# Optimization experiments

Measured on AMD Instinct MI355X. Metric: run time of the kernel, lower is better.

## Reference

```python
import jax, jax.numpy as jnp
import numpy as np
from jax import lax

B, C, H, W = 1, 128, 56, 56
NH, NG, KS = 4, 1, 3
CG = C // NG          # channels per group
CH = C // NH          # channels per head
NHG = NH // NG        # heads per group
SCALE = CH ** -0.5


def _norm_grid(h, w, n):
    # matches _get_normalized_grid: (y, x) order, each normalized to [-1, 1]
    y = jnp.arange(h, dtype=jnp.float32) / (h - 1.0) * 2.0 - 1.0
    x = jnp.arange(w, dtype=jnp.float32) / (w - 1.0) * 2.0 - 1.0
    g = jnp.stack(jnp.meshgrid(y, x, indexing='ij'), axis=-1)  # (h, w, 2)
    return jnp.broadcast_to(g[None], (n, h, w, 2))


def _grid_sample(img, grid):
    # F.grid_sample: bilinear, align_corners=True, zeros padding; grid is (x, y) in [-1, 1]
    n, c, hi, wi = img.shape
    gs = grid.shape[1:-1]
    gx = grid[..., 0].reshape(n, -1)
    gy = grid[..., 1].reshape(n, -1)
    fx = (gx + 1.0) * 0.5 * (wi - 1)
    fy = (gy + 1.0) * 0.5 * (hi - 1)
    x0 = jnp.floor(fx)
    y0 = jnp.floor(fy)
    wx = fx - x0
    wy = fy - y0
    x0 = x0.astype(jnp.int32)
    y0 = y0.astype(jnp.int32)
    imgf = img.reshape(n, c, hi * wi)

    def corner(xi, yi, wgt):
        valid = (xi >= 0) & (xi < wi) & (yi >= 0) & (yi < hi)
        idx = jnp.clip(yi, 0, hi - 1) * wi + jnp.clip(xi, 0, wi - 1)
        vals = jax.vmap(lambda im, ii: jnp.take(im, ii, axis=1))(imgf, idx)  # (n, c, P)
        return vals * (wgt * valid)[:, None, :]

    out = (corner(x0, y0, (1 - wx) * (1 - wy)) + corner(x0 + 1, y0, wx * (1 - wy))
           + corner(x0, y0 + 1, (1 - wx) * wy) + corner(x0 + 1, y0 + 1, wx * wy))
    return out.reshape((n, c) + gs)


def _conv1x1(t, w, b):
    return jnp.einsum('bchw,oc->bohw', t, w) + b[None, :, None, None]


def _forward(x, query, dw_w, dw_b, ln_w, ln_b, pw_w, k_w, k_b, v_w, v_b, out_w, out_b, rpe_table):
    # conv_offset: depthwise 3x3 (stride 1, pad 1) -> channel LayerNorm -> GELU -> 1x1 to 2ch (no bias)
    qg = query.reshape(B * NG, CG, H, W)
    t = lax.conv_general_dilated(qg, dw_w, (1, 1), ((1, 1), (1, 1)),
                                 dimension_numbers=('NCHW', 'OIHW', 'NCHW'),
                                 feature_group_count=CG) + dw_b[None, :, None, None]
    mu = t.mean(axis=1, keepdims=True)
    var = ((t - mu) ** 2).mean(axis=1, keepdims=True)
    t = (t - mu) / jnp.sqrt(var + 1e-5) * ln_w[None, :, None, None] + ln_b[None, :, None, None]
    t = jax.nn.gelu(t, approximate=False)
    offset = jnp.einsum('bchw,oc->bohw', t, pw_w)  # (BG, 2, Hk, Wk) in (y, x) order
    Hk, Wk = offset.shape[-2:]
    n_sample = Hk * Wk

    # tanh-scaled offsets (scale_offset_range=True, factor 0.5)
    rng = jnp.array([1.0 / (Hk - 1.0), 1.0 / (Wk - 1.0)], jnp.float32).reshape(1, 2, 1, 1)
    offset = jnp.tanh(offset) * rng * 0.5
    offset = jnp.transpose(offset, (0, 2, 3, 1))  # (BG, Hk, Wk, 2)

    ref = _norm_grid(Hk, Wk, B * NG)
    rwo = offset + ref  # no clamp in the scale_offset_range branch

    # sample K/V features at deformed locations
    xs = _grid_sample(x.reshape(B * NG, CG, H, W), rwo[..., ::-1])  # (BG, CG, Hk, Wk)
    xs = xs.reshape(B, C, 1, n_sample)

    q = query.reshape(B * NH, CH, H * W)
    k = _conv1x1(xs, k_w, k_b).reshape(B * NH, CH, n_sample)
    v = _conv1x1(xs, v_w, v_b).reshape(B * NH, CH, n_sample)

    attn = jnp.einsum('bcm,bcn->bmn', q, k) * SCALE  # (B*NH, HW, n_sample)

    # relative position bias via bilinear lookup of rpe_table at displacements
    rpe = jnp.broadcast_to(rpe_table[None], (B,) + rpe_table.shape).reshape(B * NG, NHG, 2 * H - 1, 2 * W - 1)
    qgrid = _norm_grid(H, W, B * NG)
    disp = (qgrid.reshape(B * NG, H * W, 2)[:, :, None, :]
            - rwo.reshape(B * NG, n_sample, 2)[:, None, :, :]) * 0.5  # (BG, HW, n_sample, 2)
    bias = _grid_sample(rpe, disp[..., ::-1]).reshape(B * NH, H * W, n_sample)

    attn = jax.nn.softmax(attn + bias, axis=2)
    out = jnp.einsum('bmn,bcn->bcm', attn, v).reshape(B, C, H, W)
    return _conv1x1(out, out_w, out_b)


def setup_inputs() -> dict:
    key = jax.random.key(0)
    ks = jax.random.split(key, 8)
    f = lambda k, sh, s=0.02: jax.random.normal(k, sh, jnp.float32) * s
    return {
        'x': jax.random.normal(ks[0], (B, C, H, W), jnp.float32),
        'query': jax.random.normal(ks[1], (B, C, H, W), jnp.float32),
        'dw_w': f(ks[2], (CG, 1, KS, KS)),
        'dw_b': jnp.zeros((CG,), jnp.float32),
        'ln_w': jnp.ones((CG,), jnp.float32),
        'ln_b': jnp.zeros((CG,), jnp.float32),
        'pw_w': f(ks[3], (2, CG)),
        'k_w': f(ks[4], (C, C)),
        'k_b': jnp.zeros((C,), jnp.float32),
        'v_w': f(ks[5], (C, C)),
        'v_b': jnp.zeros((C,), jnp.float32),
        'out_w': f(ks[6], (C, C)),
        'out_b': jnp.zeros((C,), jnp.float32),
        'rpe_table': f(ks[7], (NH, 2 * H - 1, 2 * W - 1), 0.01),
    }


def reference(x, query, dw_w, dw_b, ln_w, ln_b, pw_w, k_w, k_b, v_w, v_b, out_w, out_b, rpe_table):
    return _forward(x, query, dw_w, dw_b, ln_w, ln_b, pw_w, k_w, k_b, v_w, v_b, out_w, out_b, rpe_table)
```

## Files before the change

### kernel.cpp

```cpp
#include <hip/hip_runtime.h>
#include <hip/hip_bf16.h>
#include <math.h>

#define HH 56
#define WW 56
#define HW 3136
#define NHEAD 4
#define RP 111
#define TP 113
#define TPE 12769
#define SCALE 0.17677669529663687f
#define LOG2E 1.44269504088896f
#define QSC (SCALE * LOG2E)
#define GHW 12544
#define NCHUNK 14
#define CLEN 224
#define NSTEP 7

typedef unsigned short ushortT;
typedef __attribute__((ext_vector_type(8))) short short8v;
typedef __attribute__((ext_vector_type(16))) float f32x16;

#define OFF_RWO  0u
#define OFF_AA   8192u
#define OFF_W4   12288u
#define OFF_KBF  24832u
#define OFF_VBF  225536u
#define OFF_QBF  426240u
#define OFF_KWT  1028352u
#define OFF_VWT  1044736u
#define OFF_OWT  1061120u
#define OFF_XT   1077504u
#define OFF_QT   1478912u
#define OFF_TP2  1880320u
#define OFF_PART 1982976u

__device__ __forceinline__ ushortT f2bf(float f) {
    unsigned u = __float_as_uint(f);
    u += 0x7fffu + ((u >> 16) & 1u);
    return (ushortT)(u >> 16);
}

__device__ __forceinline__ unsigned cvtpk(float lo, float hi) {
    unsigned r;
    asm("v_cvt_pk_bf16_f32 %0, %1, %2" : "=v"(r) : "v"(lo), "v"(hi));
    return r;
}

__device__ __forceinline__ float fexp2(float x) {
    float r;
    asm("v_exp_f32 %0, %1" : "=v"(r) : "v"(x));
    return r;
}

__global__ __launch_bounds__(256) void prep_all_kernel(
    const float* __restrict__ kw, const float* __restrict__ vw, const float* __restrict__ ow,
    const float* __restrict__ rpe, const float* __restrict__ x, const float* __restrict__ query,
    float* __restrict__ kwT, float* __restrict__ vwT, float* __restrict__ owT,
    float2* __restrict__ tp2, float* __restrict__ xT, float* __restrict__ qT,
    ushortT* __restrict__ qbf) {
    const int job = blockIdx.y;
    __shared__ float tile[32][33];
    if (job < 3) {
        int i = blockIdx.x * 256 + threadIdx.x;
        if (i >= 16384) return;
        const float* srcw = (job == 0) ? kw : (job == 1) ? vw : ow;
        float* dstw       = (job == 0) ? kwT : (job == 1) ? vwT : owT;
        dstw[(i & 127) * 128 + (i >> 7)] = srcw[i];
    } else if (job == 3) {
        int i = blockIdx.x * 256 + threadIdx.x;
        if (i >= NHEAD * TPE) return;
        int hd = i / TPE, r = i % TPE;
        int py = r / TP, px = r % TP;
        float v0 = 0.f, v1 = 0.f;
        if (py >= 1 && py <= RP) {
            if (px >= 1 && px <= RP) v0 = rpe[hd * RP * RP + (py - 1) * RP + (px - 1)] * LOG2E;
            if (px <= RP - 1)        v1 = rpe[hd * RP * RP + (py - 1) * RP + px] * LOG2E;
        }
        tp2[i] = make_float2(v0, v1);
    } else {
        int bx = blockIdx.x;
        if (bx >= 392) return;
        const float* src = (job == 5) ? query : x;
        float* dst       = (job == 5) ? qT : xT;
        int pt = (bx % 98) * 32, ct = (bx / 98) * 32;
        int jj = threadIdx.x & 31, ii = threadIdx.x >> 5;
#pragma unroll
        for (int r = 0; r < 4; r++)
            tile[ii + r * 8][jj] = src[(ct + ii + r * 8) * HW + pt + jj];
        __syncthreads();
#pragma unroll
        for (int r = 0; r < 4; r++) {
            int p = pt + ii + r * 8, cc = ct + jj;
            float val = tile[jj][ii + r * 8];
            dst[p * 128 + cc] = val;
            if (job == 5)
                qbf[(size_t)((cc >> 5) * HW + p) * 32 + (cc & 31)] = f2bf(val * QSC);
        }
    }
}

__device__ __forceinline__ float wave_sum(float v) {
#pragma unroll
    for (int o = 1; o < 64; o <<= 1) v += __shfl_xor(v, o);
    return v;
}

__global__ __launch_bounds__(128) void offset_kernel(
    const float* __restrict__ qT, const float* __restrict__ dww, const float* __restrict__ dwb,
    const float* __restrict__ lnw, const float* __restrict__ lnb, const float* __restrict__ pww,
    float* __restrict__ rwo, int* __restrict__ aa, float* __restrict__ w4) {
    int p = blockIdx.x;
    int c = threadIdx.x;
    int h = p / WW, w = p % WW;

    float t = dwb[c];
#pragma unroll
    for (int ky = 0; ky < 3; ky++) {
        int yy = h + ky - 1;
        if ((unsigned)yy < (unsigned)HH) {
#pragma unroll
            for (int kx = 0; kx < 3; kx++) {
                int xx = w + kx - 1;
                if ((unsigned)xx < (unsigned)WW)
                    t += qT[(yy * WW + xx) * 128 + c] * dww[c * 9 + ky * 3 + kx];
            }
        }
    }

    __shared__ float sred[4];
    int wid = c >> 6, lane0 = ((c & 63) == 0);

    float s = wave_sum(t);
    if (lane0) sred[wid] = s;
    __syncthreads();
    float mu = (sred[0] + sred[1]) * (1.f / 128.f);
    float d = t - mu;
    __syncthreads();
    s = wave_sum(d * d);
    if (lane0) sred[wid] = s;
    __syncthreads();
    float var = (sred[0] + sred[1]) * (1.f / 128.f);

    float tn = d / sqrtf(var + 1e-5f) * lnw[c] + lnb[c];
    float g = 0.5f * tn * (1.f + erff(tn * 0.70710678118654752f));

    float sy = wave_sum(g * pww[c]);
    float sx = wave_sum(g * pww[128 + c]);
    __syncthreads();
    if (lane0) { sred[wid] = sy; sred[2 + wid] = sx; }
    __syncthreads();
    if (c == 0) {
        float thy = tanhf(sred[0] + sred[1]);
        float thx = tanhf(sred[2] + sred[3]);
        rwo[p * 2]     = thy * (0.5f / 55.f) + ((float)h * (2.f / 55.f) - 1.f);
        rwo[p * 2 + 1] = thx * (0.5f / 55.f) + ((float)w * (2.f / 55.f) - 1.f);
        float ty = 55.f - (float)h - 0.25f * thy;
        float tx = 55.f - (float)w - 0.25f * thx;
        float tyf = floorf(ty), txf = floorf(tx);
        float wy = ty - tyf, wx = tx - txf;
        aa[p] = ((int)tyf) * TP + (int)txf + TP + 1;
        float4 wv;
        wv.x = (1.f - wx) * (1.f - wy);
        wv.y = wx * (1.f - wy);
        wv.z = (1.f - wx) * wy;
        wv.w = wx * wy;
        ((float4*)w4)[p] = wv;
    }
}

__global__ __launch_bounds__(128) void sample_kv_kernel(
    const float* __restrict__ xT, const float* __restrict__ rwo,
    const float* __restrict__ kwT, const float* __restrict__ vwT,
    const float* __restrict__ kb, const float* __restrict__ vb,
    ushortT* __restrict__ kbf, ushortT* __restrict__ vbf) {
    int n0 = blockIdx.x * 8;
    int tid = threadIdx.x;

    __shared__ float xs[128 * 9];
    __shared__ int   cidx[8][4];
    __shared__ float cw[8][4];
    __shared__ ushortT kst[8][128];

    if (tid < 8) {
        int n = n0 + tid;
        float gy = rwo[2 * n], gx = rwo[2 * n + 1];
        float fx = (gx + 1.f) * 27.5f;
        float fy = (gy + 1.f) * 27.5f;
        float x0f = floorf(fx), y0f = floorf(fy);
        float wx = fx - x0f, wy = fy - y0f;
        int x0 = (int)x0f, y0 = (int)y0f;
#pragma unroll
        for (int k = 0; k < 4; k++) {
            int xi = x0 + (k & 1), yi = y0 + (k >> 1);
            float wgt = ((k & 1) ? wx : 1.f - wx) * ((k >> 1) ? wy : 1.f - wy);
            bool v = (xi >= 0) && (xi < WW) && (yi >= 0) && (yi < HH);
            cidx[tid][k] = min(max(yi, 0), HH - 1) * WW + min(max(xi, 0), WW - 1);
            cw[tid][k] = v ? wgt : 0.f;
        }
    }
    __syncthreads();

#pragma unroll
    for (int j = 0; j < 8; j++) {
        float s = cw[j][0] * xT[cidx[j][0] * 128 + tid]
                + cw[j][1] * xT[cidx[j][1] * 128 + tid]
                + cw[j][2] * xT[cidx[j][2] * 128 + tid]
                + cw[j][3] * xT[cidx[j][3] * 128 + tid];
        xs[tid * 9 + j] = s;
    }
    __syncthreads();

    float ak[8], av[8];
#pragma unroll
    for (int j = 0; j < 8; j++) { ak[j] = 0.f; av[j] = 0.f; }
    for (int c = 0; c < 128; c++) {
        float wk = kwT[c * 128 + tid];
        float wv = vwT[c * 128 + tid];
#pragma unroll
        for (int j = 0; j < 8; j++) {
            float xv = xs[c * 9 + j];
            ak[j] += wk * xv;
            av[j] += wv * xv;
        }
    }
    float kbv = kb[tid], vbv = vb[tid];
    int hh = tid >> 5, ch = tid & 31;

    unsigned vp[4];
#pragma unroll
    for (int q = 0; q < 4; q++)
        vp[q] = (unsigned)f2bf(av[2 * q] + vbv) | ((unsigned)f2bf(av[2 * q + 1] + vbv) << 16);
    *(uint4*)(vbf + (size_t)(hh * 32 + ch) * HW + n0) = make_uint4(vp[0], vp[1], vp[2], vp[3]);

#pragma unroll
    for (int j = 0; j < 8; j++) kst[j][tid] = f2bf(ak[j] + kbv);
    __syncthreads();
#pragma unroll
    for (int r = 0; r < 4; r++) {
        int lin = tid + 128 * r;
        int j = lin >> 6, dd = lin & 63;
        int o = 2 * dd;
        unsigned val = *(unsigned*)&kst[j][o];
        int hd2 = o >> 5, ch2 = o & 31;
        ((unsigned*)kbf)[((size_t)(hd2 * HW + n0 + j) * 32 + ch2) >> 1] = val;
    }
}

__device__ __forceinline__ void mkw(float pa0, float pa1, float pb0, float pb1, int h,
                                    unsigned &wlo, unsigned &whi) {
    float ta0 = __shfl_xor(pa0, 32);
    float ta1 = __shfl_xor(pa1, 32);
    float tb0 = __shfl_xor(pb0, 32);
    float tb1 = __shfl_xor(pb1, 32);
    wlo = cvtpk(h ? tb0 : pa0, h ? tb1 : pa1);
    whi = cvtpk(h ? pb0 : ta0, h ? pb1 : ta1);
}

__global__ __launch_bounds__(128) void attn_kernel(
    const ushortT* __restrict__ qbf, const ushortT* __restrict__ kbf,
    const ushortT* __restrict__ vbf,
    const int* __restrict__ aa, const float4* __restrict__ w4,
    const float2* __restrict__ tp2g, float* __restrict__ part) {
    const int chunk = blockIdx.x;
    const int mtile = blockIdx.y;
    const int hd = blockIdx.z;
    const int tid = threadIdx.x;
    const int wv = tid >> 6;
    const int l = tid & 63;
    const int lm = l & 31;
    const int h = l >> 5;

    const int start = chunk * CLEN;
    const int mg = mtile * 64 + wv * 32 + lm;

    __shared__ int aa_s[CLEN];
    __shared__ float4 w4_s[CLEN];
    __shared__ float ubuf[12 * TP * 2];
    __shared__ int sred[4];
    float2* tpw = (float2*)ubuf;
    float* obuf = ubuf;

    int rmin = 1 << 20, rmax = -(1 << 20);
    for (int i = tid; i < CLEN; i += 128) {
        int av = aa[start + i];
        aa_s[i] = av;
        w4_s[i] = w4[start + i];
        int row = (av * 37118) >> 22;
        rmin = min(rmin, row);
        rmax = max(rmax, row);
    }
#pragma unroll
    for (int o = 1; o < 64; o <<= 1) {
        rmin = min(rmin, __shfl_xor(rmin, o));
        rmax = max(rmax, __shfl_xor(rmax, o));
    }
    if (l == 0) { sred[wv] = rmin; sred[2 + wv] = rmax; }
    __syncthreads();
    rmin = min(sred[0], sred[1]);
    rmax = max(sred[2], sred[3]);
    const int rm0 = (mtile * 64) / WW;
    const int rm1 = (mtile * 64 + 63) / WW;
    const int R0 = rmin + rm0;
    const int NR = rmax + rm1 + 2 - R0;

    const float2* srcw = tp2g + hd * TPE + R0 * TP;
    for (int i = tid; i < NR * TP; i += 128) tpw[i] = srcw[i];
    const int rbase = R0 * TP;
    for (int i = tid; i < CLEN; i += 128) aa_s[i] -= rbase;
    __syncthreads();

    const int base_m = (mg / WW) * TP + (mg % WW);

    const ushortT* qb = qbf + (size_t)(hd * HW + mg) * 32 + h * 8;
    short8v qf0 = *(const short8v*)(qb);
    short8v qf1 = *(const short8v*)(qb + 16);

    const ushortT* kbp = kbf + (size_t)(hd * HW + start) * 32;
    const ushortT* vbp = vbf + (size_t)(hd * 32 + lm) * HW + start;

    f32x16 accO;
#pragma unroll
    for (int i = 0; i < 16; i++) accO[i] = 0.f;
    float ssum = 0.f;

    for (int nt = 0; nt < NSTEP; ++nt) {
        const ushortT* ka = kbp + (size_t)(nt * 32 + lm) * 32 + h * 8;
        short8v kf0 = *(const short8v*)(ka);
        short8v kf1 = *(const short8v*)(ka + 16);
        f32x16 s;
#pragma unroll
        for (int i = 0; i < 16; i++) s[i] = 0.f;
        s = __builtin_amdgcn_mfma_f32_32x32x16_bf16(kf0, qf0, s, 0, 0, 0);
        s = __builtin_amdgcn_mfma_f32_32x32x16_bf16(kf1, qf1, s, 0, 0, 0);

        float p[16];
#pragma unroll
        for (int r = 0; r < 16; ++r) {
            int nl = nt * 32 + (r & 3) + 8 * (r >> 2) + 4 * h;
            int a0 = aa_s[nl] + base_m;
            float4 wvv = w4_s[nl];
            float2 t01 = tpw[a0];
            float2 t23 = tpw[a0 + TP];
            float bias = wvv.x * t01.x + wvv.y * t01.y + wvv.z * t23.x + wvv.w * t23.y;
            float pr = fexp2(s[r] + bias);
            ssum += pr;
            p[r] = pr;
        }

        union { unsigned u[4]; short8v s8; } A0, A1;
        mkw(p[0], p[1], p[4], p[5], h, A0.u[0], A0.u[2]);
        mkw(p[2], p[3], p[6], p[7], h, A0.u[1], A0.u[3]);
        mkw(p[8], p[9], p[12], p[13], h, A1.u[0], A1.u[2]);
        mkw(p[10], p[11], p[14], p[15], h, A1.u[1], A1.u[3]);

        const ushortT* va = vbp + nt * 32 + h * 8;
        short8v vf0 = *(const short8v*)(va);
        short8v vf1 = *(const short8v*)(va + 16);
        accO = __builtin_amdgcn_mfma_f32_32x32x16_bf16(A0.s8, vf0, accO, 0, 0, 0);
        accO = __builtin_amdgcn_mfma_f32_32x32x16_bf16(A1.s8, vf1, accO, 0, 0, 0);
    }

    float st = ssum + __shfl_xor(ssum, 32);

    __syncthreads();
#pragma unroll
    for (int r = 0; r < 16; ++r) {
        int mr = (r & 3) + 8 * (r >> 2) + 4 * h;
        obuf[(wv * 32 + mr) * 33 + lm] = accO[r];
    }
    __syncthreads();

    float* pbase = part + (size_t)(chunk * 33) * GHW + hd * HW;
    if (h == 0) pbase[mg] = st;
    int c0 = h * 16;
#pragma unroll
    for (int k = 0; k < 4; ++k) {
        float4 o4 = *(const float4*)&obuf[(wv * 32 + lm) * 33 + c0 + 4 * k];
        pbase[(size_t)(1 + c0 + 4 * k + 0) * GHW + mg] = o4.x;
        pbase[(size_t)(1 + c0 + 4 * k + 1) * GHW + mg] = o4.y;
        pbase[(size_t)(1 + c0 + 4 * k + 2) * GHW + mg] = o4.z;
        pbase[(size_t)(1 + c0 + 4 * k + 3) * GHW + mg] = o4.w;
    }
}

__global__ __launch_bounds__(128) void combine_out_kernel(
    const float* __restrict__ part, const float* __restrict__ owT,
    const float* __restrict__ ob, float* __restrict__ out) {
    int m0 = blockIdx.x * 8;
    int tid = threadIdx.x;
    int hd = tid >> 5, c = tid & 31;

    __shared__ float at[128 * 9];
    __shared__ float inv_s[4][8];

    float a[8];
#pragma unroll
    for (int j = 0; j < 8; j++) a[j] = 0.f;
    for (int k = 0; k < NCHUNK; k++) {
        const float* p = part + (size_t)(k * 33 + 1 + c) * GHW + hd * HW + m0;
        float4 x0 = *(const float4*)p, x1 = *(const float4*)(p + 4);
        a[0] += x0.x; a[1] += x0.y; a[2] += x0.z; a[3] += x0.w;
        a[4] += x1.x; a[5] += x1.y; a[6] += x1.z; a[7] += x1.w;
    }
    if (c == 0) {
        float sm[8];
#pragma unroll
        for (int j = 0; j < 8; j++) sm[j] = 0.f;
        for (int k = 0; k < NCHUNK; k++) {
            const float* p = part + (size_t)(k * 33) * GHW + hd * HW + m0;
            float4 x0 = *(const float4*)p, x1 = *(const float4*)(p + 4);
            sm[0] += x0.x; sm[1] += x0.y; sm[2] += x0.z; sm[3] += x0.w;
            sm[4] += x1.x; sm[5] += x1.y; sm[6] += x1.z; sm[7] += x1.w;
        }
#pragma unroll
        for (int j = 0; j < 8; j++) inv_s[hd][j] = 1.f / sm[j];
    }
    __syncthreads();
#pragma unroll
    for (int j = 0; j < 8; j++) at[tid * 9 + j] = a[j] * inv_s[hd][j];
    __syncthreads();

    float acc[8];
#pragma unroll
    for (int j = 0; j < 8; j++) acc[j] = 0.f;
    for (int cc = 0; cc < 128; cc++) {
        float w = owT[cc * 128 + tid];
#pragma unroll
        for (int j = 0; j < 8; j++) acc[j] += w * at[cc * 9 + j];
    }
    float b = ob[tid];
#pragma unroll
    for (int j = 0; j < 8; j++) out[tid * HW + m0 + j] = acc[j] + b;
}

extern "C" void kernel_launch(void* const* d_in, const int* in_sizes, int n_in,
                              void* d_out, int out_size, void* d_ws, size_t ws_size,
                              hipStream_t stream) {
    const float* x     = (const float*)d_in[0];
    const float* query = (const float*)d_in[1];
    const float* dww   = (const float*)d_in[2];
    const float* dwb   = (const float*)d_in[3];
    const float* lnw   = (const float*)d_in[4];
    const float* lnb   = (const float*)d_in[5];
    const float* pww   = (const float*)d_in[6];
    const float* kw    = (const float*)d_in[7];
    const float* kb    = (const float*)d_in[8];
    const float* vw    = (const float*)d_in[9];
    const float* vb    = (const float*)d_in[10];
    const float* ow    = (const float*)d_in[11];
    const float* ob    = (const float*)d_in[12];
    const float* rpe   = (const float*)d_in[13];
    float* out = (float*)d_out;
    float* ws  = (float*)d_ws;

    prep_all_kernel<<<dim3(392, 6), 256, 0, stream>>>(
        kw, vw, ow, rpe, x, query,
        ws + OFF_KWT, ws + OFF_VWT, ws + OFF_OWT, (float2*)(ws + OFF_TP2),
        ws + OFF_XT, ws + OFF_QT, (ushortT*)(ws + OFF_QBF));
    offset_kernel<<<HW, 128, 0, stream>>>(ws + OFF_QT, dww, dwb, lnw, lnb, pww,
                                          ws + OFF_RWO, (int*)(ws + OFF_AA), ws + OFF_W4);
    sample_kv_kernel<<<392, 128, 0, stream>>>(ws + OFF_XT, ws + OFF_RWO,
                                              ws + OFF_KWT, ws + OFF_VWT, kb, vb,
                                              (ushortT*)(ws + OFF_KBF), (ushortT*)(ws + OFF_VBF));
    attn_kernel<<<dim3(NCHUNK, 49, NHEAD), 128, 0, stream>>>(
        (const ushortT*)(ws + OFF_QBF), (const ushortT*)(ws + OFF_KBF),
        (const ushortT*)(ws + OFF_VBF),
        (const int*)(ws + OFF_AA), (const float4*)(ws + OFF_W4),
        (const float2*)(ws + OFF_TP2), ws + OFF_PART);
    combine_out_kernel<<<392, 128, 0, stream>>>(ws + OFF_PART, ws + OFF_OWT, ob, out);
}
```

Measured before the change: 168.6 us.

## Accumulate split-K attention partials with atomics instead of per-chunk partial buffers

```diff
diff --git a/kernel.cpp b/kernel.cpp
--- a/kernel.cpp
+++ b/kernel.cpp
@@ -15,6 +15,7 @@
 #define GHW 12544
 #define NCHUNK 14
 #define CLEN 224
+#define BLEN 448
 #define NSTEP 7
 
 typedef unsigned short ushortT;
@@ -33,7 +34,8 @@
 #define OFF_XT   1077504u
 #define OFF_QT   1478912u
 #define OFF_TP2  1880320u
-#define OFF_PART 1982976u
+#define OFF_ATT2 1982976u
+#define OFF_SUM  2384384u
 
 __device__ __forceinline__ ushortT f2bf(float f) {
     unsigned u = __float_as_uint(f);
@@ -257,57 +259,42 @@
     whi = cvtpk(h ? pb0 : ta0, h ? pb1 : ta1);
 }
 
-__global__ __launch_bounds__(128) void attn_kernel(
+__global__ __launch_bounds__(256) void attn_kernel(
     const ushortT* __restrict__ qbf, const ushortT* __restrict__ kbf,
     const ushortT* __restrict__ vbf,
     const int* __restrict__ aa, const float4* __restrict__ w4,
-    const float2* __restrict__ tp2g, float* __restrict__ part) {
-    const int chunk = blockIdx.x;
+    const float2* __restrict__ tp2g, float* __restrict__ att2, float* __restrict__ sums) {
+    const int bx = blockIdx.x;
     const int mtile = blockIdx.y;
     const int hd = blockIdx.z;
     const int tid = threadIdx.x;
     const int wv = tid >> 6;
+    const int msub = wv & 1;
+    const int csub = wv >> 1;
     const int l = tid & 63;
     const int lm = l & 31;
     const int h = l >> 5;
 
-    const int start = chunk * CLEN;
-    const int mg = mtile * 64 + wv * 32 + lm;
-
-    __shared__ int aa_s[CLEN];
-    __shared__ float4 w4_s[CLEN];
-    __shared__ float ubuf[12 * TP * 2];
-    __shared__ int sred[4];
-    float2* tpw = (float2*)ubuf;
-    float* obuf = ubuf;
-
-    int rmin = 1 << 20, rmax = -(1 << 20);
-    for (int i = tid; i < CLEN; i += 128) {
-        int av = aa[start + i];
-        aa_s[i] = av;
-        w4_s[i] = w4[start + i];
-        int row = (av * 37118) >> 22;
-        rmin = min(rmin, row);
-        rmax = max(rmax, row);
-    }
-#pragma unroll
-    for (int o = 1; o < 64; o <<= 1) {
-        rmin = min(rmin, __shfl_xor(rmin, o));
-        rmax = max(rmax, __shfl_xor(rmax, o));
-    }
-    if (l == 0) { sred[wv] = rmin; sred[2 + wv] = rmax; }
-    __syncthreads();
-    rmin = min(sred[0], sred[1]);
-    rmax = max(sred[2], sred[3]);
-    const int rm0 = (mtile * 64) / WW;
-    const int rm1 = (mtile * 64 + 63) / WW;
-    const int R0 = rmin + rm0;
-    const int NR = rmax + rm1 + 2 - R0;
-
-    const float2* srcw = tp2g + hd * TPE + R0 * TP;
-    for (int i = tid; i < NR * TP; i += 128) tpw[i] = srcw[i];
+    const int N0 = bx * BLEN;
+    const int m0 = mtile * 64;
+    const int mg = m0 + msub * 32 + lm;
+
+    __shared__ int aa_s[BLEN];
+    __shared__ float4 w4_s[BLEN];
+    __shared__ float2 tpw[12 * TP];
+
+    const int h_min = N0 / WW;
+    const int rm0 = m0 / WW, rm1 = (m0 + 63) / WW;
+    const int R0 = 48 - h_min + rm0;
+    const int NR = 10 + rm1 - rm0;
     const int rbase = R0 * TP;
-    for (int i = tid; i < CLEN; i += 128) aa_s[i] -= rbase;
+
+    const float2* srcw = tp2g + hd * TPE + rbase;
+    for (int i = tid; i < NR * TP; i += 256) tpw[i] = srcw[i];
+    for (int i = tid; i < BLEN; i += 256) {
+        aa_s[i] = aa[N0 + i] - rbase;
+        w4_s[i] = w4[N0 + i];
+    }
     __syncthreads();
 
     const int base_m = (mg / WW) * TP + (mg % WW);
@@ -316,8 +303,9 @@
     short8v qf0 = *(const short8v*)(qb);
     short8v qf1 = *(const short8v*)(qb + 16);
 
-    const ushortT* kbp = kbf + (size_t)(hd * HW + start) * 32;
-    const ushortT* vbp = vbf + (size_t)(hd * 32 + lm) * HW + start;
+    const int nwave = N0 + csub * CLEN;
+    const ushortT* kbp = kbf + (size_t)(hd * HW + nwave) * 32;
+    const ushortT* vbp = vbf + (size_t)(hd * 32 + lm) * HW + nwave;
 
     f32x16 accO;
 #pragma unroll
@@ -337,7 +325,7 @@
         float p[16];
 #pragma unroll
         for (int r = 0; r < 16; ++r) {
-            int nl = nt * 32 + (r & 3) + 8 * (r >> 2) + 4 * h;
+            int nl = csub * CLEN + nt * 32 + (r & 3) + 8 * (r >> 2) + 4 * h;
             int a0 = aa_s[nl] + base_m;
             float4 wvv = w4_s[nl];
             float2 t01 = tpw[a0];
@@ -361,32 +349,19 @@
         accO = __builtin_amdgcn_mfma_f32_32x32x16_bf16(A1.s8, vf1, accO, 0, 0, 0);
     }
 
-    float st = ssum + __shfl_xor(ssum, 32);
-
-    __syncthreads();
+    float* abase = att2 + (size_t)(hd * HW + m0 + msub * 32) * 32 + lm;
 #pragma unroll
     for (int r = 0; r < 16; ++r) {
         int mr = (r & 3) + 8 * (r >> 2) + 4 * h;
-        obuf[(wv * 32 + mr) * 33 + lm] = accO[r];
-    }
-    __syncthreads();
-
-    float* pbase = part + (size_t)(chunk * 33) * GHW + hd * HW;
-    if (h == 0) pbase[mg] = st;
-    int c0 = h * 16;
-#pragma unroll
-    for (int k = 0; k < 4; ++k) {
-        float4 o4 = *(const float4*)&obuf[(wv * 32 + lm) * 33 + c0 + 4 * k];
-        pbase[(size_t)(1 + c0 + 4 * k + 0) * GHW + mg] = o4.x;
-        pbase[(size_t)(1 + c0 + 4 * k + 1) * GHW + mg] = o4.y;
-        pbase[(size_t)(1 + c0 + 4 * k + 2) * GHW + mg] = o4.z;
-        pbase[(size_t)(1 + c0 + 4 * k + 3) * GHW + mg] = o4.w;
-    }
+        atomicAdd(abase + (size_t)mr * 32, accO[r]);
+    }
+    float st = ssum + __shfl_xor(ssum, 32);
+    if (h == 0) atomicAdd(&sums[hd * HW + mg], st);
 }
 
 __global__ __launch_bounds__(128) void combine_out_kernel(
-    const float* __restrict__ part, const float* __restrict__ owT,
-    const float* __restrict__ ob, float* __restrict__ out) {
+    const float* __restrict__ att2, const float* __restrict__ sums,
+    const float* __restrict__ owT, const float* __restrict__ ob, float* __restrict__ out) {
     int m0 = blockIdx.x * 8;
     int tid = threadIdx.x;
     int hd = tid >> 5, c = tid & 31;
@@ -394,31 +369,15 @@
     __shared__ float at[128 * 9];
     __shared__ float inv_s[4][8];
 
-    float a[8];
-#pragma unroll
-    for (int j = 0; j < 8; j++) a[j] = 0.f;
-    for (int k = 0; k < NCHUNK; k++) {
-        const float* p = part + (size_t)(k * 33 + 1 + c) * GHW + hd * HW + m0;
-        float4 x0 = *(const float4*)p, x1 = *(const float4*)(p + 4);
-        a[0] += x0.x; a[1] += x0.y; a[2] += x0.z; a[3] += x0.w;
-        a[4] += x1.x; a[5] += x1.y; a[6] += x1.z; a[7] += x1.w;
-    }
-    if (c == 0) {
-        float sm[8];
-#pragma unroll
-        for (int j = 0; j < 8; j++) sm[j] = 0.f;
-        for (int k = 0; k < NCHUNK; k++) {
-            const float* p = part + (size_t)(k * 33) * GHW + hd * HW + m0;
-            float4 x0 = *(const float4*)p, x1 = *(const float4*)(p + 4);
-            sm[0] += x0.x; sm[1] += x0.y; sm[2] += x0.z; sm[3] += x0.w;
-            sm[4] += x1.x; sm[5] += x1.y; sm[6] += x1.z; sm[7] += x1.w;
-        }
-#pragma unroll
-        for (int j = 0; j < 8; j++) inv_s[hd][j] = 1.f / sm[j];
-    }
-    __syncthreads();
-#pragma unroll
-    for (int j = 0; j < 8; j++) at[tid * 9 + j] = a[j] * inv_s[hd][j];
+    if (tid < 32) {
+        int hh = tid >> 3, j = tid & 7;
+        inv_s[hh][j] = 1.f / sums[hh * HW + m0 + j];
+    }
+    __syncthreads();
+
+#pragma unroll
+    for (int j = 0; j < 8; j++)
+        at[tid * 9 + j] = att2[(size_t)(hd * HW + m0 + j) * 32 + c] * inv_s[hd][j];
     __syncthreads();
 
     float acc[8];
@@ -463,10 +422,12 @@
     sample_kv_kernel<<<392, 128, 0, stream>>>(ws + OFF_XT, ws + OFF_RWO,
                                               ws + OFF_KWT, ws + OFF_VWT, kb, vb,
                                               (ushortT*)(ws + OFF_KBF), (ushortT*)(ws + OFF_VBF));
-    attn_kernel<<<dim3(NCHUNK, 49, NHEAD), 128, 0, stream>>>(
+    hipMemsetAsync(ws + OFF_ATT2, 0, (size_t)(401408 + 12544) * 4, stream);
+    attn_kernel<<<dim3(7, 49, NHEAD), 256, 0, stream>>>(
         (const ushortT*)(ws + OFF_QBF), (const ushortT*)(ws + OFF_KBF),
         (const ushortT*)(ws + OFF_VBF),
         (const int*)(ws + OFF_AA), (const float4*)(ws + OFF_W4),
-        (const float2*)(ws + OFF_TP2), ws + OFF_PART);
-    combine_out_kernel<<<392, 128, 0, stream>>>(ws + OFF_PART, ws + OFF_OWT, ob, out);
-}
+        (const float2*)(ws + OFF_TP2), ws + OFF_ATT2, ws + OFF_SUM);
+    combine_out_kernel<<<392, 128, 0, stream>>>(ws + OFF_ATT2, ws + OFF_SUM,
+                                                ws + OFF_OWT, ob, out);
+}
```

Result: faster. 162.5 us (-3.7%).
